# Performance work log

Measured on AMD Instinct MI355X. Metric: run time of the kernel, lower is better.

The kernel has to match this reference:

```python
import jax, jax.numpy as jnp
import numpy as np

VOCAB = 23
PAD_IDX = 21
SOS_IDX = 22
LATENT = 128
COND = 16
HID = 1024
EMB = 512
MAX_LEN = 64
B = 4096


def setup_inputs() -> dict:
    key = jax.random.key(0)
    ks = jax.random.split(key, 12)
    s = lambda *d: 1.0 / np.sqrt(d[-1])
    inp = {
        "z": jax.random.normal(ks[0], (B, LATENT), jnp.float32),
        "cond": jax.random.normal(ks[1], (B, COND), jnp.float32),
        "emb_table": jax.random.normal(ks[2], (VOCAB, EMB), jnp.float32),
        "W_lh": jax.random.uniform(ks[3], (HID, LATENT + COND), jnp.float32, -s(LATENT + COND), s(LATENT + COND)),
        "b_lh": jax.random.uniform(ks[4], (HID,), jnp.float32, -s(LATENT + COND), s(LATENT + COND)),
        "W_ih": jax.random.uniform(ks[5], (4 * HID, EMB), jnp.float32, -s(HID), s(HID)),
        "W_hh": jax.random.uniform(ks[6], (4 * HID, HID), jnp.float32, -s(HID), s(HID)),
        "b_ih": jax.random.uniform(ks[7], (4 * HID,), jnp.float32, -s(HID), s(HID)),
        "b_hh": jax.random.uniform(ks[8], (4 * HID,), jnp.float32, -s(HID), s(HID)),
        "W_out": jax.random.uniform(ks[9], (VOCAB, HID), jnp.float32, -s(HID), s(HID)),
        "b_out": jax.random.uniform(ks[10], (VOCAB,), jnp.float32, -s(HID), s(HID)),
    }
    return inp


def reference(z, cond, emb_table, W_lh, b_lh, W_ih, W_hh, b_ih, b_hh, W_out, b_out):
    # padding_idx row of the embedding is zero (and non-trainable in torch)
    E = emb_table.at[PAD_IDX].set(0.0)
    # initial hidden from latent+cond; initial cell is zeros
    h0 = jnp.concatenate([z, cond], axis=1) @ W_lh.T + b_lh          # [B, H]
    c0 = jnp.zeros_like(h0)
    x0 = E[jnp.full((z.shape[0],), SOS_IDX, dtype=jnp.int32)]        # [B, E]
    bias = b_ih + b_hh

    def step(carry, _):
        h, c, x = carry
        gates = x @ W_ih.T + h @ W_hh.T + bias                        # [B, 4H]
        i, f, g, o = jnp.split(gates, 4, axis=1)
        i = jax.nn.sigmoid(i)
        f = jax.nn.sigmoid(f)
        g = jnp.tanh(g)
        o = jax.nn.sigmoid(o)
        c = f * c + i * g
        h = o * jnp.tanh(c)
        logits = h @ W_out.T + b_out                                  # [B, V]
        nxt = jnp.argmax(logits, axis=1)                              # greedy token
        x = E[nxt]
        return (h, c, x), logits

    _, logits_t = jax.lax.scan(step, (h0, c0, x0), None, length=MAX_LEN)  # [T, B, V]
    return jnp.transpose(logits_t, (1, 0, 2))                         # [B, T, V]
```

## Files before the change

kernel.cpp:

```cpp
#include <hip/hip_runtime.h>

#define NB 4096
#define NH 1024
#define NE 512
#define NV 23
#define NT 64
#define NL 144
#define PADV 21
#define SOSV 22

typedef unsigned short u16;
typedef __attribute__((ext_vector_type(4))) float f32x4;
typedef __attribute__((ext_vector_type(8))) __bf16 bf16x8;
typedef __attribute__((ext_vector_type(8))) unsigned short u16x8;

__device__ __forceinline__ u16 f2bf(float x) {
  unsigned u = __float_as_uint(x);
  u += 0x7FFFu + ((u >> 16) & 1u);
  return (u16)(u >> 16);
}
__device__ __forceinline__ float bf2f(u16 h) {
  return __uint_as_float(((unsigned)h) << 16);
}

__device__ __forceinline__ size_t hidx(int m, int j) {
  return ((size_t)(((m >> 8) * 32 + (j >> 5)) * 4 + ((j >> 3) & 3)) * 2048)
         + (size_t)((m & 255) * 8) + (j & 7);
}

__global__ void prep_kernel(const float* __restrict__ Whh, u16* __restrict__ Whi,
                            u16* __restrict__ Wlo, float* __restrict__ c,
                            int* __restrict__ tok) {
  int i = blockIdx.x * 256 + threadIdx.x;
  float wv = Whh[i];
  u16 hi = f2bf(wv);
  u16 lo = f2bf(wv - bf2f(hi));
  const int nw = i >> 10, k = i & 1023;
  const int g = nw >> 10, jcol = nw & 1023;
  const int jt = jcol >> 6, jl = jcol & 63;
  const int row = ((jl >> 4) << 6) + (g << 4) + (jl & 15);
  const size_t oi = ((size_t)((jt * 32 + (k >> 5)) * 4 + ((k >> 3) & 3)) * 2048)
                    + (size_t)(row * 8) + (k & 7);
  Whi[oi] = hi;
  Wlo[oi] = lo;
  c[i] = 0.0f;
  if (i < NB) tok[i] = SOSV;
}

__global__ void exw_kernel(const float* __restrict__ emb, const float* __restrict__ Wih,
                           const float* __restrict__ bih, const float* __restrict__ bhh,
                           float* __restrict__ ExW) {
  __shared__ float Es[NE];
  const int v = blockIdx.y;
  const int n = blockIdx.x * 256 + threadIdx.x;
  for (int k = threadIdx.x; k < NE; k += 256)
    Es[k] = (v == PADV) ? 0.0f : emb[v * NE + k];
  __syncthreads();
  float s = bih[n] + bhh[n];
  const float* wr = Wih + (long)n * NE;
  for (int k = 0; k < NE; ++k) s = fmaf(Es[k], wr[k], s);
  ExW[v * (4 * NH) + n] = s;
}

__global__ void h0_kernel(const float* __restrict__ z, const float* __restrict__ cnd,
                          const float* __restrict__ Wlh, const float* __restrict__ blh,
                          u16* __restrict__ hhi, u16* __restrict__ hlo) {
  __shared__ float zc[8][NL];
  const int b0 = blockIdx.y * 8;
  const int j = blockIdx.x * 256 + threadIdx.x;
  for (int idx = threadIdx.x; idx < 8 * NL; idx += 256) {
    int bi = idx / NL, k = idx % NL;
    zc[bi][k] = (k < 128) ? z[(long)(b0 + bi) * 128 + k]
                          : cnd[(long)(b0 + bi) * 16 + (k - 128)];
  }
  __syncthreads();
  float acc[8];
  const float bj = blh[j];
#pragma unroll
  for (int bi = 0; bi < 8; ++bi) acc[bi] = bj;
  const float* wr = Wlh + (long)j * NL;
  for (int k = 0; k < NL; ++k) {
    float wv = wr[k];
#pragma unroll
    for (int bi = 0; bi < 8; ++bi) acc[bi] = fmaf(wv, zc[bi][k], acc[bi]);
  }
#pragma unroll
  for (int bi = 0; bi < 8; ++bi) {
    size_t idx = hidx(b0 + bi, j);
    u16 hi = f2bf(acc[bi]);
    hhi[idx] = hi;
    hlo[idx] = f2bf(acc[bi] - bf2f(hi));
  }
}

__device__ __forceinline__ void stage8(const u16* __restrict__ src, u16* dst) {
#pragma unroll
  for (int i = 0; i < 8; ++i)
    __builtin_amdgcn_global_load_lds(
        (const __attribute__((address_space(1))) void*)(src + i * 512),
        (__attribute__((address_space(3))) void*)(dst + i * 512), 16, 0, 0);
}

__global__ __launch_bounds__(512, 2)
void gates_cell_kernel(const u16* __restrict__ Whi, const u16* __restrict__ Wlo,
                       const u16* __restrict__ hhi_in, const u16* __restrict__ hlo_in,
                       const float* __restrict__ ExW, const int* __restrict__ tok,
                       float* __restrict__ c, u16* __restrict__ hhi_out,
                       u16* __restrict__ hlo_out) {
  __shared__ u16 lds[65536];

  const int bid = blockIdx.x;
  const int swz = (bid & 7) * 32 + (bid >> 3);
  const int jt = swz >> 4;
  const int mt = swz & 15;
  const int m0 = mt << 8;
  const int j0 = jt << 6;

  const int tid = threadIdx.x;
  const int w = tid >> 6, l = tid & 63;
  const int wm = w >> 1, wn = w & 1;
  const int q = l >> 4, rL = l & 15;

  const int mat = w >> 1, hf = w & 1;
  const u16* simg = (mat == 0) ? hhi_in : (mat == 1) ? hlo_in : (mat == 2) ? Whi : Wlo;
  const size_t sbase = ((mat < 2) ? ((size_t)mt * 262144) : ((size_t)jt * 262144))
                       + (size_t)hf * 4096 + (size_t)l * 8;
  const u16* sit = simg + sbase;
  u16* dwave = (u16*)lds + mat * 16384 + hf * 4096;

  f32x4 acc[4][8];
#pragma unroll
  for (int mi = 0; mi < 4; ++mi)
#pragma unroll
    for (int ni = 0; ni < 8; ++ni) acc[mi][ni] = (f32x4){0.f, 0.f, 0.f, 0.f};

  const int qoff = q * 2048 + rL * 8;

  stage8(sit, dwave);
  __syncthreads();

  int buf = 0;
  for (int ks = 0; ks < 32; ++ks) {
    if (ks < 31) stage8(sit + (size_t)(ks + 1) * 8192, dwave + (buf ^ 1) * 8192);

    bf16x8 ah[4], al[4];
    const u16* ab = lds + buf * 8192 + qoff + wm * 512;
#pragma unroll
    for (int mi = 0; mi < 4; ++mi) {
      ah[mi] = *reinterpret_cast<const bf16x8*>(ab + mi * 128);
      al[mi] = *reinterpret_cast<const bf16x8*>(ab + 16384 + mi * 128);
    }
    const u16* bb = lds + 32768 + buf * 8192 + qoff + wn * 1024;
#pragma unroll
    for (int ni = 0; ni < 8; ++ni) {
      const bf16x8 bh = *reinterpret_cast<const bf16x8*>(bb + ni * 128);
      const bf16x8 bl = *reinterpret_cast<const bf16x8*>(bb + 16384 + ni * 128);
#pragma unroll
      for (int mi = 0; mi < 4; ++mi)
        acc[mi][ni] = __builtin_amdgcn_mfma_f32_16x16x32_bf16(ah[mi], bh, acc[mi][ni], 0, 0, 0);
#pragma unroll
      for (int mi = 0; mi < 4; ++mi)
        acc[mi][ni] = __builtin_amdgcn_mfma_f32_16x16x32_bf16(ah[mi], bl, acc[mi][ni], 0, 0, 0);
#pragma unroll
      for (int mi = 0; mi < 4; ++mi)
        acc[mi][ni] = __builtin_amdgcn_mfma_f32_16x16x32_bf16(al[mi], bh, acc[mi][ni], 0, 0, 0);
    }
    __syncthreads();
    buf ^= 1;
  }

#pragma unroll
  for (int mi = 0; mi < 4; ++mi) {
#pragma unroll
    for (int r = 0; r < 4; ++r) {
      const int m = m0 + wm * 64 + mi * 16 + q * 4 + r;
      const int tk = tok[m];
      const float* exr = ExW + (size_t)tk * 4096;
#pragma unroll
      for (int jh = 0; jh < 2; ++jh) {
        const int j = j0 + (wn * 2 + jh) * 16 + rL;
        const float gi = acc[mi][jh * 4 + 0][r] + exr[j];
        const float gf = acc[mi][jh * 4 + 1][r] + exr[NH + j];
        const float gg = acc[mi][jh * 4 + 2][r] + exr[2 * NH + j];
        const float go = acc[mi][jh * 4 + 3][r] + exr[3 * NH + j];
        const float i_ = 1.0f / (1.0f + expf(-gi));
        const float f_ = 1.0f / (1.0f + expf(-gf));
        const float g_ = tanhf(gg);
        const float o_ = 1.0f / (1.0f + expf(-go));
        const size_t cidx = (size_t)m * NH + j;
        const float cn = f_ * c[cidx] + i_ * g_;
        c[cidx] = cn;
        const float hn = o_ * tanhf(cn);
        const u16 hi = f2bf(hn);
        const size_t oidx = hidx(m, j);
        hhi_out[oidx] = hi;
        hlo_out[oidx] = f2bf(hn - bf2f(hi));
      }
    }
  }
}

__global__ __launch_bounds__(256)
void logits_kernel(const u16* __restrict__ hhi, const u16* __restrict__ hlo,
                   const float* __restrict__ Wout, const float* __restrict__ bout,
                   float* __restrict__ out, int* __restrict__ tok, int t) {
  __shared__ float hs[4][NH];
  __shared__ float part[8][24][4];
  __shared__ float lg[4][24];
  const int b0 = blockIdx.x * 4;
  const int tid = threadIdx.x;
  for (int ci = tid; ci < 512; ci += 256) {
    const int bi = ci >> 7, cj = ci & 127;
    const int m = b0 + bi;
    const int ks = cj >> 2, qq = cj & 3;
    const size_t base = ((size_t)(((m >> 8) * 32 + ks) * 4 + qq) * 2048)
                        + (size_t)((m & 255) * 8);
    const u16x8 vh = *reinterpret_cast<const u16x8*>(hhi + base);
    const u16x8 vl = *reinterpret_cast<const u16x8*>(hlo + base);
    const int kb = ks * 32 + qq * 8;
#pragma unroll
    for (int e = 0; e < 8; ++e) hs[bi][kb + e] = bf2f(vh[e]) + bf2f(vl[e]);
  }
  __syncthreads();
  const int v = tid & 31, kc = tid >> 5;
  if (v < NV) {
    float s0 = 0.f, s1 = 0.f, s2 = 0.f, s3 = 0.f;
    const float* wr = Wout + (long)v * NH + kc * 128;
    const int kb = kc * 128;
    for (int k = 0; k < 128; ++k) {
      float wv = wr[k];
      s0 = fmaf(wv, hs[0][kb + k], s0);
      s1 = fmaf(wv, hs[1][kb + k], s1);
      s2 = fmaf(wv, hs[2][kb + k], s2);
      s3 = fmaf(wv, hs[3][kb + k], s3);
    }
    part[kc][v][0] = s0; part[kc][v][1] = s1;
    part[kc][v][2] = s2; part[kc][v][3] = s3;
  }
  __syncthreads();
  if (tid < NV * 4) {
    const int vv = tid >> 2, bi = tid & 3;
    float s = bout[vv];
#pragma unroll
    for (int k = 0; k < 8; ++k) s += part[k][vv][bi];
    lg[bi][vv] = s;
    out[((long)(b0 + bi) * NT + t) * NV + vv] = s;
  }
  __syncthreads();
  if (tid < 4) {
    float best = lg[tid][0];
    int bv = 0;
    for (int vv = 1; vv < NV; ++vv) {
      float x = lg[tid][vv];
      if (x > best) { best = x; bv = vv; }
    }
    tok[b0 + tid] = bv;
  }
}

extern "C" void kernel_launch(void* const* d_in, const int* in_sizes, int n_in,
                              void* d_out, int out_size, void* d_ws, size_t ws_size,
                              hipStream_t stream) {
  const float* z    = (const float*)d_in[0];
  const float* cnd  = (const float*)d_in[1];
  const float* emb  = (const float*)d_in[2];
  const float* Wlh  = (const float*)d_in[3];
  const float* blh  = (const float*)d_in[4];
  const float* Wih  = (const float*)d_in[5];
  const float* Whh  = (const float*)d_in[6];
  const float* bih  = (const float*)d_in[7];
  const float* bhh  = (const float*)d_in[8];
  const float* Wout = (const float*)d_in[9];
  const float* bout = (const float*)d_in[10];
  float* out = (float*)d_out;

  char* ws = (char*)d_ws;
  size_t off = 0;
  auto alloc = [&](size_t bytes) -> void* {
    off = (off + 255) & ~(size_t)255;
    void* p = ws + off;
    off += bytes;
    return p;
  };
  u16* Whi = (u16*)alloc((size_t)4 * NH * NH * 2);
  u16* Wlo = (u16*)alloc((size_t)4 * NH * NH * 2);
  float* ExW = (float*)alloc((size_t)NV * 4 * NH * 4);
  u16* hhi0 = (u16*)alloc((size_t)NB * NH * 2);
  u16* hhi1 = (u16*)alloc((size_t)NB * NH * 2);
  u16* hlo0 = (u16*)alloc((size_t)NB * NH * 2);
  u16* hlo1 = (u16*)alloc((size_t)NB * NH * 2);
  float* cbuf = (float*)alloc((size_t)NB * NH * 4);
  int* tokb = (int*)alloc((size_t)NB * 4);
  u16* hhi[2] = {hhi0, hhi1};
  u16* hlo[2] = {hlo0, hlo1};

  prep_kernel<<<dim3((4 * NH * NH) / 256), dim3(256), 0, stream>>>(Whh, Whi, Wlo, cbuf, tokb);
  exw_kernel<<<dim3((4 * NH) / 256, NV), dim3(256), 0, stream>>>(emb, Wih, bih, bhh, ExW);
  h0_kernel<<<dim3(NH / 256, NB / 8), dim3(256), 0, stream>>>(z, cnd, Wlh, blh, hhi[0], hlo[0]);

  int p = 0;
  for (int t = 0; t < NT; ++t) {
    gates_cell_kernel<<<dim3(256), dim3(512), 0, stream>>>(
        Whi, Wlo, hhi[p], hlo[p], ExW, tokb, cbuf, hhi[p ^ 1], hlo[p ^ 1]);
    logits_kernel<<<dim3(NB / 4), dim3(256), 0, stream>>>(
        hhi[p ^ 1], hlo[p ^ 1], Wout, bout, out, tokb, t);
    p ^= 1;
  }
}
```

Measured before the change: 6.583 ms.

## Interleave async LDS staging with MFMA phases and batch 8 rows per logits block

The gates kernel's K loop is split into four phases. The next tile's global-to-LDS loads are spread across those phases, with explicit barriers, sched_barrier fences and setprio around the MFMA bursts, and a single vmcnt wait at the end of each iteration. The point is to overlap memory staging with matrix math and cut stalls at the barriers. Token indices are prefetched into registers before the main loop, and the logits kernel now handles 8 batch rows per block instead of 4 so each Wout row read is reused more. The risks are more barriers per iteration and higher register pressure.

```diff
diff --git a/kernel.cpp b/kernel.cpp
--- a/kernel.cpp
+++ b/kernel.cpp
@@ -93,12 +93,10 @@
   }
 }
 
-__device__ __forceinline__ void stage8(const u16* __restrict__ src, u16* dst) {
-#pragma unroll
-  for (int i = 0; i < 8; ++i)
-    __builtin_amdgcn_global_load_lds(
-        (const __attribute__((address_space(1))) void*)(src + i * 512),
-        (__attribute__((address_space(3))) void*)(dst + i * 512), 16, 0, 0);
+__device__ __forceinline__ void stage1(const u16* __restrict__ src, u16* dst, int i) {
+  __builtin_amdgcn_global_load_lds(
+      (const __attribute__((address_space(1))) void*)(src + i * 512),
+      (__attribute__((address_space(3))) void*)(dst + i * 512), 16, 0, 0);
 }
 
 __global__ __launch_bounds__(512, 2)
@@ -128,6 +126,13 @@
   const u16* sit = simg + sbase;
   u16* dwave = (u16*)lds + mat * 16384 + hf * 4096;
 
+  int tkv[16];
+#pragma unroll
+  for (int mi = 0; mi < 4; ++mi)
+#pragma unroll
+    for (int r = 0; r < 4; ++r)
+      tkv[mi * 4 + r] = tok[m0 + wm * 64 + mi * 16 + q * 4 + r];
+
   f32x4 acc[4][8];
 #pragma unroll
   for (int mi = 0; mi < 4; ++mi)
@@ -136,36 +141,69 @@
 
   const int qoff = q * 2048 + rL * 8;
 
-  stage8(sit, dwave);
-  __syncthreads();
+#pragma unroll
+  for (int i = 0; i < 8; ++i) stage1(sit, dwave, i);
+  asm volatile("s_waitcnt vmcnt(0)" ::: "memory");
+  __builtin_amdgcn_s_barrier();
+  __builtin_amdgcn_sched_barrier(0);
 
   int buf = 0;
   for (int ks = 0; ks < 32; ++ks) {
-    if (ks < 31) stage8(sit + (size_t)(ks + 1) * 8192, dwave + (buf ^ 1) * 8192);
-
+    const u16* ab = lds + buf * 8192 + qoff + wm * 512;
+    const u16* bb = lds + 32768 + buf * 8192 + qoff + wn * 1024;
+    const u16* snext = sit + (size_t)(ks + 1) * 8192;
+    u16* dnext = dwave + (buf ^ 1) * 8192;
     bf16x8 ah[4], al[4];
-    const u16* ab = lds + buf * 8192 + qoff + wm * 512;
-#pragma unroll
-    for (int mi = 0; mi < 4; ++mi) {
-      ah[mi] = *reinterpret_cast<const bf16x8*>(ab + mi * 128);
-      al[mi] = *reinterpret_cast<const bf16x8*>(ab + 16384 + mi * 128);
-    }
-    const u16* bb = lds + 32768 + buf * 8192 + qoff + wn * 1024;
-#pragma unroll
-    for (int ni = 0; ni < 8; ++ni) {
-      const bf16x8 bh = *reinterpret_cast<const bf16x8*>(bb + ni * 128);
-      const bf16x8 bl = *reinterpret_cast<const bf16x8*>(bb + 16384 + ni * 128);
-#pragma unroll
-      for (int mi = 0; mi < 4; ++mi)
-        acc[mi][ni] = __builtin_amdgcn_mfma_f32_16x16x32_bf16(ah[mi], bh, acc[mi][ni], 0, 0, 0);
-#pragma unroll
-      for (int mi = 0; mi < 4; ++mi)
-        acc[mi][ni] = __builtin_amdgcn_mfma_f32_16x16x32_bf16(ah[mi], bl, acc[mi][ni], 0, 0, 0);
-#pragma unroll
-      for (int mi = 0; mi < 4; ++mi)
-        acc[mi][ni] = __builtin_amdgcn_mfma_f32_16x16x32_bf16(al[mi], bh, acc[mi][ni], 0, 0, 0);
-    }
-    __syncthreads();
+
+#pragma unroll
+    for (int ph = 0; ph < 4; ++ph) {
+      if (ph == 0) {
+#pragma unroll
+        for (int mi = 0; mi < 4; ++mi) {
+          ah[mi] = *reinterpret_cast<const bf16x8*>(ab + mi * 128);
+          al[mi] = *reinterpret_cast<const bf16x8*>(ab + 16384 + mi * 128);
+        }
+      }
+      bf16x8 bh0 = *reinterpret_cast<const bf16x8*>(bb + (2 * ph + 0) * 128);
+      bf16x8 bl0 = *reinterpret_cast<const bf16x8*>(bb + 16384 + (2 * ph + 0) * 128);
+      bf16x8 bh1 = *reinterpret_cast<const bf16x8*>(bb + (2 * ph + 1) * 128);
+      bf16x8 bl1 = *reinterpret_cast<const bf16x8*>(bb + 16384 + (2 * ph + 1) * 128);
+      if (ks < 31) {
+        if (ph == 0) { stage1(snext, dnext, 0); stage1(snext, dnext, 1); stage1(snext, dnext, 2); }
+        if (ph == 1) { stage1(snext, dnext, 3); stage1(snext, dnext, 4); stage1(snext, dnext, 5); }
+        if (ph == 2) { stage1(snext, dnext, 6); stage1(snext, dnext, 7); }
+      }
+      __builtin_amdgcn_sched_barrier(0);
+      __builtin_amdgcn_s_barrier();
+      __builtin_amdgcn_sched_barrier(0);
+      __builtin_amdgcn_s_setprio(1);
+#pragma unroll
+      for (int mi = 0; mi < 4; ++mi)
+        acc[mi][2 * ph + 0] = __builtin_amdgcn_mfma_f32_16x16x32_bf16(ah[mi], bh0, acc[mi][2 * ph + 0], 0, 0, 0);
+#pragma unroll
+      for (int mi = 0; mi < 4; ++mi)
+        acc[mi][2 * ph + 0] = __builtin_amdgcn_mfma_f32_16x16x32_bf16(ah[mi], bl0, acc[mi][2 * ph + 0], 0, 0, 0);
+#pragma unroll
+      for (int mi = 0; mi < 4; ++mi)
+        acc[mi][2 * ph + 0] = __builtin_amdgcn_mfma_f32_16x16x32_bf16(al[mi], bh0, acc[mi][2 * ph + 0], 0, 0, 0);
+#pragma unroll
+      for (int mi = 0; mi < 4; ++mi)
+        acc[mi][2 * ph + 1] = __builtin_amdgcn_mfma_f32_16x16x32_bf16(ah[mi], bh1, acc[mi][2 * ph + 1], 0, 0, 0);
+#pragma unroll
+      for (int mi = 0; mi < 4; ++mi)
+        acc[mi][2 * ph + 1] = __builtin_amdgcn_mfma_f32_16x16x32_bf16(ah[mi], bl1, acc[mi][2 * ph + 1], 0, 0, 0);
+#pragma unroll
+      for (int mi = 0; mi < 4; ++mi)
+        acc[mi][2 * ph + 1] = __builtin_amdgcn_mfma_f32_16x16x32_bf16(al[mi], bh1, acc[mi][2 * ph + 1], 0, 0, 0);
+      __builtin_amdgcn_s_setprio(0);
+      __builtin_amdgcn_sched_barrier(0);
+    }
+
+    if (ks < 31) {
+      asm volatile("s_waitcnt vmcnt(0)" ::: "memory");
+      __builtin_amdgcn_s_barrier();
+      __builtin_amdgcn_sched_barrier(0);
+    }
     buf ^= 1;
   }
 
@@ -174,8 +212,7 @@
 #pragma unroll
     for (int r = 0; r < 4; ++r) {
       const int m = m0 + wm * 64 + mi * 16 + q * 4 + r;
-      const int tk = tok[m];
-      const float* exr = ExW + (size_t)tk * 4096;
+      const float* exr = ExW + (size_t)tkv[mi * 4 + r] * 4096;
 #pragma unroll
       for (int jh = 0; jh < 2; ++jh) {
         const int j = j0 + (wn * 2 + jh) * 16 + rL;
@@ -204,12 +241,12 @@
 void logits_kernel(const u16* __restrict__ hhi, const u16* __restrict__ hlo,
                    const float* __restrict__ Wout, const float* __restrict__ bout,
                    float* __restrict__ out, int* __restrict__ tok, int t) {
-  __shared__ float hs[4][NH];
-  __shared__ float part[8][24][4];
-  __shared__ float lg[4][24];
-  const int b0 = blockIdx.x * 4;
+  __shared__ float hs[8][NH];
+  __shared__ float part[8][24][8];
+  __shared__ float lg[8][24];
+  const int b0 = blockIdx.x * 8;
   const int tid = threadIdx.x;
-  for (int ci = tid; ci < 512; ci += 256) {
+  for (int ci = tid; ci < 1024; ci += 256) {
     const int bi = ci >> 7, cj = ci & 127;
     const int m = b0 + bi;
     const int ks = cj >> 2, qq = cj & 3;
@@ -224,22 +261,22 @@
   __syncthreads();
   const int v = tid & 31, kc = tid >> 5;
   if (v < NV) {
-    float s0 = 0.f, s1 = 0.f, s2 = 0.f, s3 = 0.f;
+    float s[8];
+#pragma unroll
+    for (int bi = 0; bi < 8; ++bi) s[bi] = 0.f;
     const float* wr = Wout + (long)v * NH + kc * 128;
     const int kb = kc * 128;
     for (int k = 0; k < 128; ++k) {
       float wv = wr[k];
-      s0 = fmaf(wv, hs[0][kb + k], s0);
-      s1 = fmaf(wv, hs[1][kb + k], s1);
-      s2 = fmaf(wv, hs[2][kb + k], s2);
-      s3 = fmaf(wv, hs[3][kb + k], s3);
-    }
-    part[kc][v][0] = s0; part[kc][v][1] = s1;
-    part[kc][v][2] = s2; part[kc][v][3] = s3;
-  }
-  __syncthreads();
-  if (tid < NV * 4) {
-    const int vv = tid >> 2, bi = tid & 3;
+#pragma unroll
+      for (int bi = 0; bi < 8; ++bi) s[bi] = fmaf(wv, hs[bi][kb + k], s[bi]);
+    }
+#pragma unroll
+    for (int bi = 0; bi < 8; ++bi) part[kc][v][bi] = s[bi];
+  }
+  __syncthreads();
+  if (tid < NV * 8) {
+    const int vv = tid >> 3, bi = tid & 7;
     float s = bout[vv];
 #pragma unroll
     for (int k = 0; k < 8; ++k) s += part[k][vv][bi];
@@ -247,7 +284,7 @@
     out[((long)(b0 + bi) * NT + t) * NV + vv] = s;
   }
   __syncthreads();
-  if (tid < 4) {
+  if (tid < 8) {
     float best = lg[tid][0];
     int bv = 0;
     for (int vv = 1; vv < NV; ++vv) {
@@ -302,7 +339,7 @@
   for (int t = 0; t < NT; ++t) {
     gates_cell_kernel<<<dim3(256), dim3(512), 0, stream>>>(
         Whi, Wlo, hhi[p], hlo[p], ExW, tokb, cbuf, hhi[p ^ 1], hlo[p ^ 1]);
-    logits_kernel<<<dim3(NB / 4), dim3(256), 0, stream>>>(
+    logits_kernel<<<dim3(NB / 8), dim3(256), 0, stream>>>(
         hhi[p ^ 1], hlo[p ^ 1], Wout, bout, out, tokb, t);
     p ^= 1;
   }
```

After: 6.330 ms. -3.8%, faster.

## Switch gate GEMM to 32x32x16 MFMA and batch 8 rows per logits block

Applied to the files above, without the earlier changes.

The recurrent gate GEMM now uses 32x32x16 bf16 MFMA tiles instead of 16x16x32. The W_hh image layout is reordered so each wave holds all four gates for one 32-column slice, and the epilogue is remapped to the 32x32 accumulator row layout. This is meant to cut LDS fragment loads per MFMA and raise matrix-core throughput. Separately, the logits kernel processes 8 batch rows per block, reusing each W_out load across more rows at the cost of more LDS and fewer blocks.

```diff
diff --git a/kernel.cpp b/kernel.cpp
--- a/kernel.cpp
+++ b/kernel.cpp
@@ -10,7 +10,7 @@
 #define SOSV 22
 
 typedef unsigned short u16;
-typedef __attribute__((ext_vector_type(4))) float f32x4;
+typedef __attribute__((ext_vector_type(16))) float f32x16;
 typedef __attribute__((ext_vector_type(8))) __bf16 bf16x8;
 typedef __attribute__((ext_vector_type(8))) unsigned short u16x8;
 
@@ -38,7 +38,7 @@
   const int nw = i >> 10, k = i & 1023;
   const int g = nw >> 10, jcol = nw & 1023;
   const int jt = jcol >> 6, jl = jcol & 63;
-  const int row = ((jl >> 4) << 6) + (g << 4) + (jl & 15);
+  const int row = g * 64 + jl;
   const size_t oi = ((size_t)((jt * 32 + (k >> 5)) * 4 + ((k >> 3) & 3)) * 2048)
                     + (size_t)(row * 8) + (k & 7);
   Whi[oi] = hi;
@@ -118,8 +118,8 @@
 
   const int tid = threadIdx.x;
   const int w = tid >> 6, l = tid & 63;
-  const int wm = w >> 1, wn = w & 1;
-  const int q = l >> 4, rL = l & 15;
+  const int wm = w >> 1, jh = w & 1;
+  const int col = l & 31, h5 = l >> 5;
 
   const int mat = w >> 1, hf = w & 1;
   const u16* simg = (mat == 0) ? hhi_in : (mat == 1) ? hlo_in : (mat == 2) ? Whi : Wlo;
@@ -128,13 +128,13 @@
   const u16* sit = simg + sbase;
   u16* dwave = (u16*)lds + mat * 16384 + hf * 4096;
 
-  f32x4 acc[4][8];
-#pragma unroll
-  for (int mi = 0; mi < 4; ++mi)
-#pragma unroll
-    for (int ni = 0; ni < 8; ++ni) acc[mi][ni] = (f32x4){0.f, 0.f, 0.f, 0.f};
-
-  const int qoff = q * 2048 + rL * 8;
+  f32x16 acc[2][4];
+#pragma unroll
+  for (int mi = 0; mi < 2; ++mi)
+#pragma unroll
+    for (int g = 0; g < 4; ++g)
+#pragma unroll
+      for (int r = 0; r < 16; ++r) acc[mi][g][r] = 0.f;
 
   stage8(sit, dwave);
   __syncthreads();
@@ -143,59 +143,63 @@
   for (int ks = 0; ks < 32; ++ks) {
     if (ks < 31) stage8(sit + (size_t)(ks + 1) * 8192, dwave + (buf ^ 1) * 8192);
 
-    bf16x8 ah[4], al[4];
-    const u16* ab = lds + buf * 8192 + qoff + wm * 512;
-#pragma unroll
-    for (int mi = 0; mi < 4; ++mi) {
-      ah[mi] = *reinterpret_cast<const bf16x8*>(ab + mi * 128);
-      al[mi] = *reinterpret_cast<const bf16x8*>(ab + 16384 + mi * 128);
-    }
-    const u16* bb = lds + 32768 + buf * 8192 + qoff + wn * 1024;
-#pragma unroll
-    for (int ni = 0; ni < 8; ++ni) {
-      const bf16x8 bh = *reinterpret_cast<const bf16x8*>(bb + ni * 128);
-      const bf16x8 bl = *reinterpret_cast<const bf16x8*>(bb + 16384 + ni * 128);
-#pragma unroll
-      for (int mi = 0; mi < 4; ++mi)
-        acc[mi][ni] = __builtin_amdgcn_mfma_f32_16x16x32_bf16(ah[mi], bh, acc[mi][ni], 0, 0, 0);
-#pragma unroll
-      for (int mi = 0; mi < 4; ++mi)
-        acc[mi][ni] = __builtin_amdgcn_mfma_f32_16x16x32_bf16(ah[mi], bl, acc[mi][ni], 0, 0, 0);
-#pragma unroll
-      for (int mi = 0; mi < 4; ++mi)
-        acc[mi][ni] = __builtin_amdgcn_mfma_f32_16x16x32_bf16(al[mi], bh, acc[mi][ni], 0, 0, 0);
+    const u16* Ah = lds + buf * 8192;
+    const u16* Al = lds + 16384 + buf * 8192;
+    const u16* Bh = lds + 32768 + buf * 8192;
+    const u16* Bl = lds + 49152 + buf * 8192;
+
+#pragma unroll
+    for (int kk = 0; kk < 2; ++kk) {
+      const int ko = (kk * 2 + h5) * 2048;
+      bf16x8 ah[2], al[2];
+#pragma unroll
+      for (int mi = 0; mi < 2; ++mi) {
+        const int ao = ko + (wm * 64 + mi * 32 + col) * 8;
+        ah[mi] = *reinterpret_cast<const bf16x8*>(Ah + ao);
+        al[mi] = *reinterpret_cast<const bf16x8*>(Al + ao);
+      }
+#pragma unroll
+      for (int g = 0; g < 4; ++g) {
+        const int bo = ko + (g * 64 + jh * 32 + col) * 8;
+        const bf16x8 bh = *reinterpret_cast<const bf16x8*>(Bh + bo);
+        const bf16x8 bl = *reinterpret_cast<const bf16x8*>(Bl + bo);
+        acc[0][g] = __builtin_amdgcn_mfma_f32_32x32x16_bf16(ah[0], bh, acc[0][g], 0, 0, 0);
+        acc[1][g] = __builtin_amdgcn_mfma_f32_32x32x16_bf16(ah[1], bh, acc[1][g], 0, 0, 0);
+        acc[0][g] = __builtin_amdgcn_mfma_f32_32x32x16_bf16(ah[0], bl, acc[0][g], 0, 0, 0);
+        acc[1][g] = __builtin_amdgcn_mfma_f32_32x32x16_bf16(ah[1], bl, acc[1][g], 0, 0, 0);
+        acc[0][g] = __builtin_amdgcn_mfma_f32_32x32x16_bf16(al[0], bh, acc[0][g], 0, 0, 0);
+        acc[1][g] = __builtin_amdgcn_mfma_f32_32x32x16_bf16(al[1], bh, acc[1][g], 0, 0, 0);
+      }
     }
     __syncthreads();
     buf ^= 1;
   }
 
-#pragma unroll
-  for (int mi = 0; mi < 4; ++mi) {
-#pragma unroll
-    for (int r = 0; r < 4; ++r) {
-      const int m = m0 + wm * 64 + mi * 16 + q * 4 + r;
+  const int j = j0 + jh * 32 + col;
+#pragma unroll
+  for (int mi = 0; mi < 2; ++mi) {
+#pragma unroll
+    for (int r = 0; r < 16; ++r) {
+      const int row = (r & 3) + ((r >> 2) << 3) + (h5 << 2);
+      const int m = m0 + wm * 64 + mi * 32 + row;
       const int tk = tok[m];
       const float* exr = ExW + (size_t)tk * 4096;
-#pragma unroll
-      for (int jh = 0; jh < 2; ++jh) {
-        const int j = j0 + (wn * 2 + jh) * 16 + rL;
-        const float gi = acc[mi][jh * 4 + 0][r] + exr[j];
-        const float gf = acc[mi][jh * 4 + 1][r] + exr[NH + j];
-        const float gg = acc[mi][jh * 4 + 2][r] + exr[2 * NH + j];
-        const float go = acc[mi][jh * 4 + 3][r] + exr[3 * NH + j];
-        const float i_ = 1.0f / (1.0f + expf(-gi));
-        const float f_ = 1.0f / (1.0f + expf(-gf));
-        const float g_ = tanhf(gg);
-        const float o_ = 1.0f / (1.0f + expf(-go));
-        const size_t cidx = (size_t)m * NH + j;
-        const float cn = f_ * c[cidx] + i_ * g_;
-        c[cidx] = cn;
-        const float hn = o_ * tanhf(cn);
-        const u16 hi = f2bf(hn);
-        const size_t oidx = hidx(m, j);
-        hhi_out[oidx] = hi;
-        hlo_out[oidx] = f2bf(hn - bf2f(hi));
-      }
+      const float gi = acc[mi][0][r] + exr[j];
+      const float gf = acc[mi][1][r] + exr[NH + j];
+      const float gg = acc[mi][2][r] + exr[2 * NH + j];
+      const float go = acc[mi][3][r] + exr[3 * NH + j];
+      const float i_ = 1.0f / (1.0f + expf(-gi));
+      const float f_ = 1.0f / (1.0f + expf(-gf));
+      const float g_ = tanhf(gg);
+      const float o_ = 1.0f / (1.0f + expf(-go));
+      const size_t cidx = (size_t)m * NH + j;
+      const float cn = f_ * c[cidx] + i_ * g_;
+      c[cidx] = cn;
+      const float hn = o_ * tanhf(cn);
+      const u16 hi = f2bf(hn);
+      const size_t oidx = hidx(m, j);
+      hhi_out[oidx] = hi;
+      hlo_out[oidx] = f2bf(hn - bf2f(hi));
     }
   }
 }
@@ -204,12 +208,12 @@
 void logits_kernel(const u16* __restrict__ hhi, const u16* __restrict__ hlo,
                    const float* __restrict__ Wout, const float* __restrict__ bout,
                    float* __restrict__ out, int* __restrict__ tok, int t) {
-  __shared__ float hs[4][NH];
-  __shared__ float part[8][24][4];
-  __shared__ float lg[4][24];
-  const int b0 = blockIdx.x * 4;
+  __shared__ float hs[8][NH];
+  __shared__ float part[8][24][8];
+  __shared__ float lg[8][24];
+  const int b0 = blockIdx.x * 8;
   const int tid = threadIdx.x;
-  for (int ci = tid; ci < 512; ci += 256) {
+  for (int ci = tid; ci < 1024; ci += 256) {
     const int bi = ci >> 7, cj = ci & 127;
     const int m = b0 + bi;
     const int ks = cj >> 2, qq = cj & 3;
@@ -224,22 +228,22 @@
   __syncthreads();
   const int v = tid & 31, kc = tid >> 5;
   if (v < NV) {
-    float s0 = 0.f, s1 = 0.f, s2 = 0.f, s3 = 0.f;
+    float s[8];
+#pragma unroll
+    for (int bi = 0; bi < 8; ++bi) s[bi] = 0.f;
     const float* wr = Wout + (long)v * NH + kc * 128;
     const int kb = kc * 128;
     for (int k = 0; k < 128; ++k) {
       float wv = wr[k];
-      s0 = fmaf(wv, hs[0][kb + k], s0);
-      s1 = fmaf(wv, hs[1][kb + k], s1);
-      s2 = fmaf(wv, hs[2][kb + k], s2);
-      s3 = fmaf(wv, hs[3][kb + k], s3);
+#pragma unroll
+      for (int bi = 0; bi < 8; ++bi) s[bi] = fmaf(wv, hs[bi][kb + k], s[bi]);
     }
-    part[kc][v][0] = s0; part[kc][v][1] = s1;
-    part[kc][v][2] = s2; part[kc][v][3] = s3;
-  }
-  __syncthreads();
-  if (tid < NV * 4) {
-    const int vv = tid >> 2, bi = tid & 3;
+#pragma unroll
+    for (int bi = 0; bi < 8; ++bi) part[kc][v][bi] = s[bi];
+  }
+  __syncthreads();
+  if (tid < NV * 8) {
+    const int vv = tid >> 3, bi = tid & 7;
     float s = bout[vv];
 #pragma unroll
     for (int k = 0; k < 8; ++k) s += part[k][vv][bi];
@@ -247,7 +251,7 @@
     out[((long)(b0 + bi) * NT + t) * NV + vv] = s;
   }
   __syncthreads();
-  if (tid < 4) {
+  if (tid < 8) {
     float best = lg[tid][0];
     int bv = 0;
     for (int vv = 1; vv < NV; ++vv) {
@@ -302,7 +306,7 @@
   for (int t = 0; t < NT; ++t) {
     gates_cell_kernel<<<dim3(256), dim3(512), 0, stream>>>(
         Whi, Wlo, hhi[p], hlo[p], ExW, tokb, cbuf, hhi[p ^ 1], hlo[p ^ 1]);
-    logits_kernel<<<dim3(NB / 4), dim3(256), 0, stream>>>(
+    logits_kernel<<<dim3(NB / 8), dim3(256), 0, stream>>>(
         hhi[p ^ 1], hlo[p ^ 1], Wout, bout, out, tokb, t);
     p ^= 1;
   }
```

Measured after the change: 7.182 ms. 1.09x slower.
